# Performance work log

Hardware: AMD Instinct MI355X
Metric: run time of the kernel (lower is better)

Reference implementation:

```python
import jax, jax.numpy as jnp
import numpy as np

B, LC, LQ, D = 32, 2048, 256, 256


def setup_inputs() -> dict:
    key = jax.random.key(0)
    kc, kq, kcm, kqm, kw = jax.random.split(key, 5)
    context = jax.random.normal(kc, (B, LC, D), dtype=jnp.float32)
    query = jax.random.normal(kq, (B, LQ, D), dtype=jnp.float32)
    # True = masked (matches torch masked_fill semantics)
    context_mask = jax.random.randint(kcm, (B, LC), 0, 2).astype(bool)
    query_mask = jax.random.randint(kqm, (B, LQ), 0, 2).astype(bool)
    # nn.Linear(3*dim, 1, bias=False) weight, flattened to (3D,)
    w0 = jax.random.normal(kw, (3 * D,), dtype=jnp.float32) * (1.0 / np.sqrt(3 * D))
    return {"context": context, "query": query, "context_mask": context_mask,
            "query_mask": query_mask, "w0": w0}


def reference(context, query, context_mask, query_mask, w0):
    d = context.shape[-1]
    wc, wq, wm = w0[:d], w0[d:2 * d], w0[2 * d:]
    # trilinear sim: w0 . [c, q, c*q]  ==  c.wc + q.wq + (c*wm) q^T
    sc = context @ wc                                   # (B, Lc)
    sq = query @ wq                                     # (B, Lq)
    sim = sc[:, :, None] + sq[:, None, :] + jnp.einsum(
        'bcd,bqd->bcq', context * wm, query)            # (B, Lc, Lq)
    mask = context_mask[:, :, None] | query_mask[:, None, :]
    sim = jnp.where(mask, jnp.float32(-1e30), sim)
    S = jax.nn.softmax(sim, axis=-1)                    # row softmax over Lq
    SS = jax.nn.softmax(sim, axis=1)                    # col softmax over Lc
    S = jnp.nan_to_num(S)
    SS = jnp.nan_to_num(SS)
    A = jnp.einsum('bcq,bqd->bcd', S, query)            # (B, Lc, D)
    T = jnp.einsum('bkq,bkd->bqd', SS, context)         # SS^T @ context, (B, Lq, D)
    Bmat = jnp.einsum('bcq,bqd->bcd', S, T)             # (B, Lc, D)
    return (A, Bmat)
```

## Files before the change

### kernel.cpp

```cpp
#include <hip/hip_runtime.h>

#define B_  32
#define LC_ 2048
#define LQ_ 256
#define D_  256
#define NEGH (-30000.0f)
#define MASKF (-100000.0f)

typedef _Float16 f16;
typedef _Float16 f16x4 __attribute__((ext_vector_type(4)));
typedef _Float16 f16x8 __attribute__((ext_vector_type(8)));
typedef float    f32x4 __attribute__((ext_vector_type(4)));

__global__ __launch_bounds__(256) void k_prepq(
    const float* __restrict__ qry, const float* __restrict__ w0,
    const int* __restrict__ qmask,
    f16* __restrict__ qrywm16, float* __restrict__ sqm)
{
    const int lane = threadIdx.x & 63;
    const int wave = threadIdx.x >> 6;
    const int r = blockIdx.x * 4 + wave;
    float4 v = *(const float4*)(qry + (long long)r * D_ + lane * 4);
    float4 wm = *(const float4*)(w0 + 2 * D_ + lane * 4);
    f16x4 h;
    h[0] = (f16)(v.x * wm.x); h[1] = (f16)(v.y * wm.y);
    h[2] = (f16)(v.z * wm.z); h[3] = (f16)(v.w * wm.w);
    *(f16x4*)(qrywm16 + (long long)r * D_ + lane * 4) = h;
    float4 wq = *(const float4*)(w0 + D_ + lane * 4);
    float s = v.x*wq.x + v.y*wq.y + v.z*wq.z + v.w*wq.w;
    #pragma unroll
    for (int off = 32; off > 0; off >>= 1) s += __shfl_down(s, off, 64);
    if (lane == 0) sqm[r] = qmask[r] ? MASKF : s;
}

__global__ __launch_bounds__(256) void k_tq(
    const float* __restrict__ in, f16* __restrict__ out)
{
    __shared__ float tile[64 * 65];
    const int b = blockIdx.z;
    const int r0 = blockIdx.x * 64, c0 = blockIdx.y * 64;
    const int t = threadIdx.x;
    const float* ib = in + (long long)b * LQ_ * D_;
    #pragma unroll
    for (int p = 0; p < 4; ++p) {
        int r = (t >> 4) + p * 16;
        int cb = (t & 15) * 4;
        float4 v = *(const float4*)(ib + (long long)(r0 + r) * D_ + c0 + cb);
        tile[r * 65 + cb + 0] = v.x;
        tile[r * 65 + cb + 1] = v.y;
        tile[r * 65 + cb + 2] = v.z;
        tile[r * 65 + cb + 3] = v.w;
    }
    __syncthreads();
    f16* ob = out + (long long)b * 512 * LQ_;
    #pragma unroll
    for (int p = 0; p < 4; ++p) {
        int c = (t >> 4) + p * 16;
        int rb = (t & 15) * 4;
        f16x4 h;
        h[0] = (f16)tile[(rb + 0) * 65 + c];
        h[1] = (f16)tile[(rb + 1) * 65 + c];
        h[2] = (f16)tile[(rb + 2) * 65 + c];
        h[3] = (f16)tile[(rb + 3) * 65 + c];
        *(f16x4*)(ob + (long long)(c0 + c) * LQ_ + r0 + rb) = h;
    }
}

#define LDA1 40
__global__ __launch_bounds__(512, 4) void k_g1(
    const float* __restrict__ ctx, const f16* __restrict__ qrywm16,
    const float* __restrict__ w0, const int* __restrict__ cmask,
    const float* __restrict__ sqm,
    f16* __restrict__ ctxT16, f16* __restrict__ p16, f16* __restrict__ pT16,
    float* __restrict__ rowm, float* __restrict__ rowinvl,
    float* __restrict__ pm, float* __restrict__ pl)
{
    __shared__ f16 As[128 * LDA1];
    __shared__ f16 Bs[256 * LDA1];
    __shared__ float wc_s[256];
    __shared__ float scm_s[128];
    __shared__ float rowpm[4][128], rowps[4][128];
    __shared__ float colpm[2][256], colps[2][256];
    __shared__ float rowmax_s[128], colmax_s[256];
    const int b = blockIdx.z;
    const int c0 = blockIdx.x * 128;
    const int t = threadIdx.x, lane = t & 63, wv = t >> 6;
    const int wm_off = (wv >> 2) * 64, wn_off = (wv & 3) * 64;
    const float* Ab = ctx + ((long long)b * LC_ + c0) * D_;
    const f16* Bb = qrywm16 + (long long)b * LQ_ * D_;
    const int srow = t >> 2, scg = (t & 3) * 8;
    const int td = t & 31, tcc = t >> 5;
    if (t < 256) wc_s[t] = w0[t];
    __syncthreads();
    f32x4 acc[4][4] = {};
    float scdot = 0.f;
    for (int k0 = 0; k0 < D_; k0 += 32) {
        float4 a0 = *(const float4*)(Ab + (long long)srow * D_ + k0 + scg);
        float4 a1 = *(const float4*)(Ab + (long long)srow * D_ + k0 + scg + 4);
        f16x8 ha;
        ha[0] = (f16)a0.x; ha[1] = (f16)a0.y; ha[2] = (f16)a0.z; ha[3] = (f16)a0.w;
        ha[4] = (f16)a1.x; ha[5] = (f16)a1.y; ha[6] = (f16)a1.z; ha[7] = (f16)a1.w;
        scdot += a0.x * wc_s[k0 + scg + 0] + a0.y * wc_s[k0 + scg + 1]
               + a0.z * wc_s[k0 + scg + 2] + a0.w * wc_s[k0 + scg + 3]
               + a1.x * wc_s[k0 + scg + 4] + a1.y * wc_s[k0 + scg + 5]
               + a1.z * wc_s[k0 + scg + 6] + a1.w * wc_s[k0 + scg + 7];
        *(f16x8*)(As + srow * LDA1 + scg) = ha;
        *(f16x8*)(Bs + srow * LDA1 + scg) = *(const f16x8*)(Bb + (long long)srow * D_ + k0 + scg);
        *(f16x8*)(Bs + (srow + 128) * LDA1 + scg) = *(const f16x8*)(Bb + (long long)(srow + 128) * D_ + k0 + scg);
        __syncthreads();
        f16x8 af[4], bf[4];
        #pragma unroll
        for (int i = 0; i < 4; ++i)
            af[i] = *(const f16x8*)(As + (wm_off + i * 16 + (lane & 15)) * LDA1 + (lane >> 4) * 8);
        #pragma unroll
        for (int j = 0; j < 4; ++j)
            bf[j] = *(const f16x8*)(Bs + (wn_off + j * 16 + (lane & 15)) * LDA1 + (lane >> 4) * 8);
        #pragma unroll
        for (int i = 0; i < 4; ++i)
            #pragma unroll
            for (int j = 0; j < 4; ++j)
                acc[i][j] = __builtin_amdgcn_mfma_f32_16x16x32_f16(af[i], bf[j], acc[i][j], 0, 0, 0);
        {
            f16x8 hT;
            #pragma unroll
            for (int j = 0; j < 8; ++j)
                hT[j] = As[(tcc * 8 + j) * LDA1 + td];
            *(f16x8*)(ctxT16 + ((long long)b * D_ + k0 + td) * LC_ + c0 + tcc * 8) = hT;
        }
        __syncthreads();
    }
    scdot += __shfl_xor(scdot, 1, 64);
    scdot += __shfl_xor(scdot, 2, 64);
    if ((t & 3) == 0)
        scm_s[srow] = cmask[b * LC_ + c0 + srow] ? MASKF : scdot;
    __syncthreads();
    float sqv[4];
    #pragma unroll
    for (int j = 0; j < 4; ++j)
        sqv[j] = sqm[b * LQ_ + wn_off + j * 16 + (lane & 15)];
    float scv[4][4];
    #pragma unroll
    for (int i = 0; i < 4; ++i)
        #pragma unroll
        for (int r = 0; r < 4; ++r)
            scv[i][r] = scm_s[wm_off + i * 16 + (lane >> 4) * 4 + r];
    float rmax[4][4], cmax[4];
    #pragma unroll
    for (int i = 0; i < 4; ++i)
        #pragma unroll
        for (int r = 0; r < 4; ++r) rmax[i][r] = -INFINITY;
    #pragma unroll
    for (int j = 0; j < 4; ++j) cmax[j] = -INFINITY;
    #pragma unroll
    for (int i = 0; i < 4; ++i) {
        #pragma unroll
        for (int r = 0; r < 4; ++r) {
            #pragma unroll
            for (int j = 0; j < 4; ++j) {
                float val = fmaxf(acc[i][j][r] + scv[i][r] + sqv[j], NEGH);
                float vr = (float)(f16)val;
                rmax[i][r] = fmaxf(rmax[i][r], vr);
                cmax[j]    = fmaxf(cmax[j], vr);
            }
        }
    }
    #pragma unroll
    for (int i = 0; i < 4; ++i)
        #pragma unroll
        for (int r = 0; r < 4; ++r) {
            rmax[i][r] = fmaxf(rmax[i][r], __shfl_xor(rmax[i][r], 1, 64));
            rmax[i][r] = fmaxf(rmax[i][r], __shfl_xor(rmax[i][r], 2, 64));
            rmax[i][r] = fmaxf(rmax[i][r], __shfl_xor(rmax[i][r], 4, 64));
            rmax[i][r] = fmaxf(rmax[i][r], __shfl_xor(rmax[i][r], 8, 64));
        }
    #pragma unroll
    for (int j = 0; j < 4; ++j) {
        cmax[j] = fmaxf(cmax[j], __shfl_xor(cmax[j], 16, 64));
        cmax[j] = fmaxf(cmax[j], __shfl_xor(cmax[j], 32, 64));
    }
    if ((lane & 15) == 0) {
        #pragma unroll
        for (int i = 0; i < 4; ++i)
            #pragma unroll
            for (int r = 0; r < 4; ++r)
                rowpm[wv & 3][wm_off + i * 16 + (lane >> 4) * 4 + r] = rmax[i][r];
    }
    if (lane < 16) {
        #pragma unroll
        for (int j = 0; j < 4; ++j) colpm[wv >> 2][wn_off + j * 16 + lane] = cmax[j];
    }
    __syncthreads();
    if (t < 128)
        rowmax_s[t] = fmaxf(fmaxf(rowpm[0][t], rowpm[1][t]), fmaxf(rowpm[2][t], rowpm[3][t]));
    if (t < 256)
        colmax_s[t] = fmaxf(colpm[0][t], colpm[1][t]);
    __syncthreads();
    float rmf[4][4], cmf[4];
    #pragma unroll
    for (int i = 0; i < 4; ++i)
        #pragma unroll
        for (int r = 0; r < 4; ++r)
            rmf[i][r] = rowmax_s[wm_off + i * 16 + (lane >> 4) * 4 + r];
    #pragma unroll
    for (int j = 0; j < 4; ++j) cmf[j] = colmax_s[wn_off + j * 16 + (lane & 15)];
    float rsum[4][4] = {}, csum[4] = {};
    #pragma unroll
    for (int i = 0; i < 4; ++i) {
        #pragma unroll
        for (int r = 0; r < 4; ++r) {
            int c = c0 + wm_off + i * 16 + (lane >> 4) * 4 + r;
            f16* prow = p16 + ((long long)b * LC_ + c) * LQ_ + wn_off + (lane & 15);
            #pragma unroll
            for (int j = 0; j < 4; ++j) {
                int q = wn_off + j * 16 + (lane & 15);
                float val = fmaxf(acc[i][j][r] + scv[i][r] + sqv[j], NEGH);
                float vr = (float)(f16)val;
                float er = __expf(vr - rmf[i][r]);
                f16 hp = (f16)er;
                prow[j * 16] = hp;
                pT16[((long long)b * LQ_ + q) * LC_ + c] = hp;
                rsum[i][r] += er;
                csum[j]    += __expf(vr - cmf[j]);
            }
        }
    }
    #pragma unroll
    for (int i = 0; i < 4; ++i)
        #pragma unroll
        for (int r = 0; r < 4; ++r) {
            rsum[i][r] += __shfl_xor(rsum[i][r], 1, 64);
            rsum[i][r] += __shfl_xor(rsum[i][r], 2, 64);
            rsum[i][r] += __shfl_xor(rsum[i][r], 4, 64);
            rsum[i][r] += __shfl_xor(rsum[i][r], 8, 64);
        }
    #pragma unroll
    for (int j = 0; j < 4; ++j) {
        csum[j] += __shfl_xor(csum[j], 16, 64);
        csum[j] += __shfl_xor(csum[j], 32, 64);
    }
    if ((lane & 15) == 0) {
        #pragma unroll
        for (int i = 0; i < 4; ++i)
            #pragma unroll
            for (int r = 0; r < 4; ++r)
                rowps[wv & 3][wm_off + i * 16 + (lane >> 4) * 4 + r] = rsum[i][r];
    }
    if (lane < 16) {
        #pragma unroll
        for (int j = 0; j < 4; ++j) colps[wv >> 2][wn_off + j * 16 + lane] = csum[j];
    }
    __syncthreads();
    if (t < 128) {
        float l = rowps[0][t] + rowps[1][t] + rowps[2][t] + rowps[3][t];
        rowm[b * LC_ + c0 + t]    = rowmax_s[t];
        rowinvl[b * LC_ + c0 + t] = 1.0f / l;
    }
    if (t < 256) {
        int idx = (b * 16 + blockIdx.x) * LQ_ + t;
        pm[idx] = colmax_s[t];
        pl[idx] = colps[0][t] + colps[1][t];
    }
}

__global__ __launch_bounds__(256) void k_colreduce(
    const float* __restrict__ pm, const float* __restrict__ pl,
    float* __restrict__ colm, float* __restrict__ colinvl)
{
    const int col = blockIdx.x * 256 + threadIdx.x;
    const int b = col >> 8, q = col & 255;
    float M = -INFINITY, L = 0.f;
    for (int ch = 0; ch < 16; ++ch) {
        int idx = (b * 16 + ch) * LQ_ + q;
        float m = pm[idx], l = pl[idx];
        float nM = fmaxf(M, m);
        L = L * __expf(M - nM) + l * __expf(m - nM);
        M = nM;
    }
    colm[col] = M; colinvl[col] = 1.0f / L;
}

#define LDA3 72
#define G3SPLIT 4
#define G3CHUNK (LC_ / G3SPLIT)
__global__ __launch_bounds__(256) void k_g3(
    const f16* __restrict__ ctxT16, const f16* __restrict__ pT16,
    const float* __restrict__ rowm, const float* __restrict__ colm,
    float* __restrict__ Tpart)
{
    __shared__ f16 As[128 * LDA3];
    __shared__ f16 Bs[64 * LDA3];
    __shared__ float rowm_s[G3CHUNK];
    __shared__ float colm_s[64];
    const int b = blockIdx.x;
    const int combo = blockIdx.y;
    const int qt = combo & 3, dh = combo >> 2;
    const int q0 = qt * 64, d0 = dh * 128;
    const int cbeg = blockIdx.z * G3CHUNK;
    const int t = threadIdx.x, lane = t & 63, wv = t >> 6;
    const int wm_off = (wv >> 1) * 64, wn_off = (wv & 1) * 32;
    for (int i = t; i < G3CHUNK; i += 256) rowm_s[i] = rowm[b * LC_ + cbeg + i];
    if (t < 64) colm_s[t] = colm[b * LQ_ + q0 + t];
    __syncthreads();
    const f16* Ab = ctxT16 + ((long long)b * D_ + d0) * LC_;
    const f16* Pb = pT16 + ((long long)b * LQ_ + q0) * LC_;
    const int ar = t >> 3, acg = (t & 7) * 8;
    f32x4 acc[4][2] = {};
    f16x8 ha[4], hb[2];
    #pragma unroll
    for (int p = 0; p < 4; ++p)
        ha[p] = *(const f16x8*)(Ab + (long long)(ar + p * 32) * LC_ + cbeg + acg);
    #pragma unroll
    for (int p = 0; p < 2; ++p)
        hb[p] = *(const f16x8*)(Pb + (long long)(ar + p * 32) * LC_ + cbeg + acg);
    for (int c0 = cbeg; c0 < cbeg + G3CHUNK; c0 += 64) {
        #pragma unroll
        for (int p = 0; p < 4; ++p)
            *(f16x8*)(As + (ar + p * 32) * LDA3 + acg) = ha[p];
        #pragma unroll
        for (int p = 0; p < 2; ++p) {
            float cmq = colm_s[ar + p * 32];
            f16x8 e;
            if (cmq < -29000.f) {
                #pragma unroll
                for (int j = 0; j < 8; ++j) e[j] = (f16)1.0f;
            } else {
                #pragma unroll
                for (int j = 0; j < 8; ++j)
                    e[j] = (f16)((float)hb[p][j] * __expf(rowm_s[(c0 - cbeg) + acg + j] - cmq));
            }
            *(f16x8*)(Bs + (ar + p * 32) * LDA3 + acg) = e;
        }
        if (c0 + 64 < cbeg + G3CHUNK) {
            #pragma unroll
            for (int p = 0; p < 4; ++p)
                ha[p] = *(const f16x8*)(Ab + (long long)(ar + p * 32) * LC_ + c0 + 64 + acg);
            #pragma unroll
            for (int p = 0; p < 2; ++p)
                hb[p] = *(const f16x8*)(Pb + (long long)(ar + p * 32) * LC_ + c0 + 64 + acg);
        }
        __syncthreads();
        #pragma unroll
        for (int kk = 0; kk < 64; kk += 32) {
            f16x8 af[4], bf[2];
            #pragma unroll
            for (int i = 0; i < 4; ++i)
                af[i] = *(const f16x8*)(As + (wm_off + i * 16 + (lane & 15)) * LDA3 + kk + (lane >> 4) * 8);
            #pragma unroll
            for (int j = 0; j < 2; ++j)
                bf[j] = *(const f16x8*)(Bs + (wn_off + j * 16 + (lane & 15)) * LDA3 + kk + (lane >> 4) * 8);
            #pragma unroll
            for (int i = 0; i < 4; ++i)
                #pragma unroll
                for (int j = 0; j < 2; ++j)
                    acc[i][j] = __builtin_amdgcn_mfma_f32_16x16x32_f16(af[i], bf[j], acc[i][j], 0, 0, 0);
        }
        __syncthreads();
    }
    float* Tb = Tpart + ((long long)blockIdx.z * B_ + b) * (LQ_ * D_);
    #pragma unroll
    for (int i = 0; i < 4; ++i) {
        #pragma unroll
        for (int r = 0; r < 4; ++r) {
            int d = d0 + wm_off + i * 16 + (lane >> 4) * 4 + r;
            float* orow = Tb + (long long)d * LQ_ + q0 + wn_off + (lane & 15);
            #pragma unroll
            for (int j = 0; j < 2; ++j)
                orow[j * 16] = acc[i][j][r];
        }
    }
}

__global__ __launch_bounds__(256) void k_bnorm(
    const float* __restrict__ Tpart, const float* __restrict__ colinvl,
    f16* __restrict__ Bcat)
{
    const long long i4 = ((long long)blockIdx.x * 256 + threadIdx.x) * 4;
    const int q = (int)(i4 & 255);
    const int d = (int)((i4 >> 8) & 255);
    const int b = (int)(i4 >> 16);
    float4 s = *(const float4*)(Tpart + i4);
    #pragma unroll
    for (int p = 1; p < G3SPLIT; ++p) {
        float4 v = *(const float4*)(Tpart + (long long)p * (B_ * LQ_ * D_) + i4);
        s.x += v.x; s.y += v.y; s.z += v.z; s.w += v.w;
    }
    float4 ci = *(const float4*)(colinvl + b * LQ_ + q);
    f16x4 h;
    h[0] = (f16)(s.x * ci.x); h[1] = (f16)(s.y * ci.y);
    h[2] = (f16)(s.z * ci.z); h[3] = (f16)(s.w * ci.w);
    *(f16x4*)(Bcat + (long long)b * 512 * LQ_ + (long long)(256 + d) * LQ_ + q) = h;
}

__global__ __launch_bounds__(256, 4) void k_g23(
    const f16* __restrict__ p16, const float* __restrict__ rowinvl,
    const f16* __restrict__ Bcat,
    float* __restrict__ outA, float* __restrict__ outB)
{
    __shared__ f16 As[128 * LDA1];
    __shared__ f16 Bs[128 * LDA1];
    const int b = blockIdx.z;
    const int c0 = blockIdx.x * 128, n0 = blockIdx.y * 128;
    const int t = threadIdx.x, lane = t & 63, wv = t >> 6;
    const int wm_off = (wv >> 1) * 64, wn_off = (wv & 1) * 64;
    const f16* Ab = p16 + ((long long)b * LC_ + c0) * LQ_;
    const f16* Bb = Bcat + ((long long)b * 512 + n0) * LQ_;
    const int srow = t >> 2, scg = (t & 3) * 8;
    f32x4 acc[4][4] = {};
    f16x8 ha[2], hb[2];
    #pragma unroll
    for (int p = 0; p < 2; ++p) {
        int r = srow + p * 64;
        ha[p] = *(const f16x8*)(Ab + (long long)r * LQ_ + scg);
        hb[p] = *(const f16x8*)(Bb + (long long)r * LQ_ + scg);
    }
    for (int k0 = 0; k0 < LQ_; k0 += 32) {
        #pragma unroll
        for (int p = 0; p < 2; ++p) {
            int r = srow + p * 64;
            *(f16x8*)(As + r * LDA1 + scg) = ha[p];
            *(f16x8*)(Bs + r * LDA1 + scg) = hb[p];
        }
        if (k0 + 32 < LQ_) {
            #pragma unroll
            for (int p = 0; p < 2; ++p) {
                int r = srow + p * 64;
                ha[p] = *(const f16x8*)(Ab + (long long)r * LQ_ + k0 + 32 + scg);
                hb[p] = *(const f16x8*)(Bb + (long long)r * LQ_ + k0 + 32 + scg);
            }
        }
        __syncthreads();
        f16x8 af[4], bf[4];
        #pragma unroll
        for (int i = 0; i < 4; ++i)
            af[i] = *(const f16x8*)(As + (wm_off + i * 16 + (lane & 15)) * LDA1 + (lane >> 4) * 8);
        #pragma unroll
        for (int j = 0; j < 4; ++j)
            bf[j] = *(const f16x8*)(Bs + (wn_off + j * 16 + (lane & 15)) * LDA1 + (lane >> 4) * 8);
        #pragma unroll
        for (int i = 0; i < 4; ++i)
            #pragma unroll
            for (int j = 0; j < 4; ++j)
                acc[i][j] = __builtin_amdgcn_mfma_f32_16x16x32_f16(af[i], bf[j], acc[i][j], 0, 0, 0);
        __syncthreads();
    }
    float* outp = (n0 < 256) ? outA : outB;
    const int nbase = (n0 < 256) ? n0 : (n0 - 256);
    #pragma unroll
    for (int i = 0; i < 4; ++i) {
        #pragma unroll
        for (int r = 0; r < 4; ++r) {
            int c = c0 + wm_off + i * 16 + (lane >> 4) * 4 + r;
            float ri = rowinvl[b * LC_ + c];
            float* orow = outp + ((long long)b * LC_ + c) * D_ + nbase + wn_off + (lane & 15);
            #pragma unroll
            for (int j = 0; j < 4; ++j)
                orow[j * 16] = acc[i][j][r] * ri;
        }
    }
}

extern "C" void kernel_launch(void* const* d_in, const int* in_sizes, int n_in,
                              void* d_out, int out_size, void* d_ws, size_t ws_size,
                              hipStream_t stream) {
    const float* ctx   = (const float*)d_in[0];
    const float* qry   = (const float*)d_in[1];
    const int*   cmask = (const int*)d_in[2];
    const int*   qmask = (const int*)d_in[3];
    const float* w0    = (const float*)d_in[4];
    float* out = (float*)d_out;

    char* w = (char*)d_ws;
    float* sqm     = (float*)w;  w += (long long)8192 * 4;
    float* rowm    = (float*)w;  w += (long long)65536 * 4;
    float* rowinvl = (float*)w;  w += (long long)65536 * 4;
    float* colm    = (float*)w;  w += (long long)8192 * 4;
    float* colinvl = (float*)w;  w += (long long)8192 * 4;
    float* pm      = (float*)w;  w += (long long)524288 * 4;
    float* pl      = (float*)w;  w += (long long)524288 * 4;
    f16*   p16     = (f16*)w;    w += (long long)16777216 * 2;
    f16*   pT16    = (f16*)w;    w += (long long)16777216 * 2;
    f16*   ctxT16  = (f16*)w;    w += (long long)16777216 * 2;
    f16*   qrywm16 = (f16*)w;    w += (long long)2097152 * 2;
    f16*   Bcat    = (f16*)w;    w += (long long)4194304 * 2;
    float* Tpart   = (float*)w;  w += (long long)G3SPLIT * 2097152 * 4;

    k_prepq<<<2048, 256, 0, stream>>>(qry, w0, qmask, qrywm16, sqm);
    k_tq<<<dim3(4, 4, 32), 256, 0, stream>>>(qry, Bcat);
    k_g1<<<dim3(16, 1, 32), 512, 0, stream>>>(ctx, qrywm16, w0, cmask, sqm,
        ctxT16, p16, pT16, rowm, rowinvl, pm, pl);
    k_colreduce<<<32, 256, 0, stream>>>(pm, pl, colm, colinvl);
    k_g3<<<dim3(32, 8, G3SPLIT), 256, 0, stream>>>(ctxT16, pT16, rowm, colm, Tpart);
    k_bnorm<<<2048, 256, 0, stream>>>(Tpart, colinvl, Bcat);
    k_g23<<<dim3(16, 4, 32), 256, 0, stream>>>(p16, rowinvl, Bcat,
        out, out + (long long)B_ * LC_ * D_);
}
```

Measured before the change: 312.6 us.

## Enlarge g3 and g23 tiles to 512-thread blocks with swizzled 1D grids

k_g3 now covers a 128x128 output tile with 8 waves instead of 128x64 with 4 waves. k_g23 covers 256x256 with 8 waves, each holding an 8x4 MFMA accumulator grid. Both kernels move to a 1D grid with a block-index swizzle that spreads consecutive blocks across batches and splits. The aim is more data reuse per LDS load, fewer global reloads, and better cache locality. The cost is a much larger accumulator register footprint in k_g23 (128 floats per lane), which lowers occupancy and risks spilling, plus fewer, larger blocks.

```diff
diff --git a/kernel.cpp b/kernel.cpp
--- a/kernel.cpp
+++ b/kernel.cpp
@@ -282,43 +282,43 @@
 #define LDA3 72
 #define G3SPLIT 4
 #define G3CHUNK (LC_ / G3SPLIT)
-__global__ __launch_bounds__(256) void k_g3(
+__global__ __launch_bounds__(512) void k_g3(
     const f16* __restrict__ ctxT16, const f16* __restrict__ pT16,
     const float* __restrict__ rowm, const float* __restrict__ colm,
     float* __restrict__ Tpart)
 {
     __shared__ f16 As[128 * LDA3];
-    __shared__ f16 Bs[64 * LDA3];
+    __shared__ f16 Bs[128 * LDA3];
     __shared__ float rowm_s[G3CHUNK];
-    __shared__ float colm_s[64];
-    const int b = blockIdx.x;
-    const int combo = blockIdx.y;
-    const int qt = combo & 3, dh = combo >> 2;
-    const int q0 = qt * 64, d0 = dh * 128;
-    const int cbeg = blockIdx.z * G3CHUNK;
+    __shared__ float colm_s[128];
+    const int lin = blockIdx.x;
+    const int swz = (lin & 7) * 64 + (lin >> 3);
+    const int combo = swz & 3;
+    const int split = (swz >> 2) & 3;
+    const int b = swz >> 4;
+    const int qt = combo & 1, dh = combo >> 1;
+    const int q0 = qt * 128, d0 = dh * 128;
+    const int cbeg = split * G3CHUNK;
     const int t = threadIdx.x, lane = t & 63, wv = t >> 6;
-    const int wm_off = (wv >> 1) * 64, wn_off = (wv & 1) * 32;
-    for (int i = t; i < G3CHUNK; i += 256) rowm_s[i] = rowm[b * LC_ + cbeg + i];
-    if (t < 64) colm_s[t] = colm[b * LQ_ + q0 + t];
+    const int wm_off = (wv >> 2) * 64, wn_off = (wv & 3) * 32;
+    if (t < G3CHUNK) rowm_s[t] = rowm[b * LC_ + cbeg + t];
+    if (t < 128) colm_s[t] = colm[b * LQ_ + q0 + t];
     __syncthreads();
     const f16* Ab = ctxT16 + ((long long)b * D_ + d0) * LC_;
     const f16* Pb = pT16 + ((long long)b * LQ_ + q0) * LC_;
     const int ar = t >> 3, acg = (t & 7) * 8;
     f32x4 acc[4][2] = {};
-    f16x8 ha[4], hb[2];
-    #pragma unroll
-    for (int p = 0; p < 4; ++p)
-        ha[p] = *(const f16x8*)(Ab + (long long)(ar + p * 32) * LC_ + cbeg + acg);
-    #pragma unroll
-    for (int p = 0; p < 2; ++p)
-        hb[p] = *(const f16x8*)(Pb + (long long)(ar + p * 32) * LC_ + cbeg + acg);
+    f16x8 ha[2], hb[2];
+    #pragma unroll
+    for (int p = 0; p < 2; ++p) {
+        ha[p] = *(const f16x8*)(Ab + (long long)(ar + p * 64) * LC_ + cbeg + acg);
+        hb[p] = *(const f16x8*)(Pb + (long long)(ar + p * 64) * LC_ + cbeg + acg);
+    }
     for (int c0 = cbeg; c0 < cbeg + G3CHUNK; c0 += 64) {
         #pragma unroll
-        for (int p = 0; p < 4; ++p)
-            *(f16x8*)(As + (ar + p * 32) * LDA3 + acg) = ha[p];
-        #pragma unroll
         for (int p = 0; p < 2; ++p) {
-            float cmq = colm_s[ar + p * 32];
+            *(f16x8*)(As + (ar + p * 64) * LDA3 + acg) = ha[p];
+            float cmq = colm_s[ar + p * 64];
             f16x8 e;
             if (cmq < -29000.f) {
                 #pragma unroll
@@ -328,15 +328,14 @@
                 for (int j = 0; j < 8; ++j)
                     e[j] = (f16)((float)hb[p][j] * __expf(rowm_s[(c0 - cbeg) + acg + j] - cmq));
             }
-            *(f16x8*)(Bs + (ar + p * 32) * LDA3 + acg) = e;
+            *(f16x8*)(Bs + (ar + p * 64) * LDA3 + acg) = e;
         }
         if (c0 + 64 < cbeg + G3CHUNK) {
             #pragma unroll
-            for (int p = 0; p < 4; ++p)
-                ha[p] = *(const f16x8*)(Ab + (long long)(ar + p * 32) * LC_ + c0 + 64 + acg);
-            #pragma unroll
-            for (int p = 0; p < 2; ++p)
-                hb[p] = *(const f16x8*)(Pb + (long long)(ar + p * 32) * LC_ + c0 + 64 + acg);
+            for (int p = 0; p < 2; ++p) {
+                ha[p] = *(const f16x8*)(Ab + (long long)(ar + p * 64) * LC_ + c0 + 64 + acg);
+                hb[p] = *(const f16x8*)(Pb + (long long)(ar + p * 64) * LC_ + c0 + 64 + acg);
+            }
         }
         __syncthreads();
         #pragma unroll
@@ -356,7 +355,7 @@
         }
         __syncthreads();
     }
-    float* Tb = Tpart + ((long long)blockIdx.z * B_ + b) * (LQ_ * D_);
+    float* Tb = Tpart + ((long long)split * B_ + b) * (LQ_ * D_);
     #pragma unroll
     for (int i = 0; i < 4; ++i) {
         #pragma unroll
@@ -391,67 +390,71 @@
     *(f16x4*)(Bcat + (long long)b * 512 * LQ_ + (long long)(256 + d) * LQ_ + q) = h;
 }
 
-__global__ __launch_bounds__(256, 4) void k_g23(
+#define LDA23 40
+__global__ __launch_bounds__(512) void k_g23(
     const f16* __restrict__ p16, const float* __restrict__ rowinvl,
     const f16* __restrict__ Bcat,
     float* __restrict__ outA, float* __restrict__ outB)
 {
-    __shared__ f16 As[128 * LDA1];
-    __shared__ f16 Bs[128 * LDA1];
-    const int b = blockIdx.z;
-    const int c0 = blockIdx.x * 128, n0 = blockIdx.y * 128;
+    __shared__ f16 As[256 * LDA23];
+    __shared__ f16 Bs[256 * LDA23];
+    const int lin = blockIdx.x;
+    const int swz = (lin & 7) * 64 + (lin >> 3);
+    const int cx = swz & 7;
+    const int ny = (swz >> 3) & 1;
+    const int b  = swz >> 4;
+    const int c0 = cx * 256, n0 = ny * 256;
     const int t = threadIdx.x, lane = t & 63, wv = t >> 6;
-    const int wm_off = (wv >> 1) * 64, wn_off = (wv & 1) * 64;
+    const int wm_off = (wv >> 2) * 128;
+    const int wn_off = (wv & 3) * 64;
     const f16* Ab = p16 + ((long long)b * LC_ + c0) * LQ_;
     const f16* Bb = Bcat + ((long long)b * 512 + n0) * LQ_;
     const int srow = t >> 2, scg = (t & 3) * 8;
-    f32x4 acc[4][4] = {};
+    f32x4 acc[8][4] = {};
     f16x8 ha[2], hb[2];
     #pragma unroll
     for (int p = 0; p < 2; ++p) {
-        int r = srow + p * 64;
+        int r = srow + p * 128;
         ha[p] = *(const f16x8*)(Ab + (long long)r * LQ_ + scg);
         hb[p] = *(const f16x8*)(Bb + (long long)r * LQ_ + scg);
     }
     for (int k0 = 0; k0 < LQ_; k0 += 32) {
         #pragma unroll
         for (int p = 0; p < 2; ++p) {
-            int r = srow + p * 64;
-            *(f16x8*)(As + r * LDA1 + scg) = ha[p];
-            *(f16x8*)(Bs + r * LDA1 + scg) = hb[p];
+            int r = srow + p * 128;
+            *(f16x8*)(As + r * LDA23 + scg) = ha[p];
+            *(f16x8*)(Bs + r * LDA23 + scg) = hb[p];
         }
         if (k0 + 32 < LQ_) {
             #pragma unroll
             for (int p = 0; p < 2; ++p) {
-                int r = srow + p * 64;
+                int r = srow + p * 128;
                 ha[p] = *(const f16x8*)(Ab + (long long)r * LQ_ + k0 + 32 + scg);
                 hb[p] = *(const f16x8*)(Bb + (long long)r * LQ_ + k0 + 32 + scg);
             }
         }
         __syncthreads();
-        f16x8 af[4], bf[4];
-        #pragma unroll
-        for (int i = 0; i < 4; ++i)
-            af[i] = *(const f16x8*)(As + (wm_off + i * 16 + (lane & 15)) * LDA1 + (lane >> 4) * 8);
+        f16x8 bf[4];
         #pragma unroll
         for (int j = 0; j < 4; ++j)
-            bf[j] = *(const f16x8*)(Bs + (wn_off + j * 16 + (lane & 15)) * LDA1 + (lane >> 4) * 8);
-        #pragma unroll
-        for (int i = 0; i < 4; ++i)
+            bf[j] = *(const f16x8*)(Bs + (wn_off + j * 16 + (lane & 15)) * LDA23 + (lane >> 4) * 8);
+        #pragma unroll
+        for (int i = 0; i < 8; ++i) {
+            f16x8 af = *(const f16x8*)(As + (wm_off + i * 16 + (lane & 15)) * LDA23 + (lane >> 4) * 8);
             #pragma unroll
             for (int j = 0; j < 4; ++j)
-                acc[i][j] = __builtin_amdgcn_mfma_f32_16x16x32_f16(af[i], bf[j], acc[i][j], 0, 0, 0);
-        __syncthreads();
-    }
-    float* outp = (n0 < 256) ? outA : outB;
-    const int nbase = (n0 < 256) ? n0 : (n0 - 256);
-    #pragma unroll
-    for (int i = 0; i < 4; ++i) {
+                acc[i][j] = __builtin_amdgcn_mfma_f32_16x16x32_f16(af, bf[j], acc[i][j], 0, 0, 0);
+        }
+        __syncthreads();
+    }
+    float* outp = (n0 == 0) ? outA : outB;
+    #pragma unroll
+    for (int i = 0; i < 8; ++i) {
         #pragma unroll
         for (int r = 0; r < 4; ++r) {
             int c = c0 + wm_off + i * 16 + (lane >> 4) * 4 + r;
             float ri = rowinvl[b * LC_ + c];
-            float* orow = outp + ((long long)b * LC_ + c) * D_ + nbase + wn_off + (lane & 15);
+            float* orow = outp + ((long long)b * LC_ + c) * D_ + wn_off + (lane & 15);
             #pragma unroll
             for (int j = 0; j < 4; ++j)
                 orow[j * 16] = acc[i][j][r] * ri;
@@ -489,8 +492,8 @@
     k_g1<<<dim3(16, 1, 32), 512, 0, stream>>>(ctx, qrywm16, w0, cmask, sqm,
         ctxT16, p16, pT16, rowm, rowinvl, pm, pl);
     k_colreduce<<<32, 256, 0, stream>>>(pm, pl, colm, colinvl);
-    k_g3<<<dim3(32, 8, G3SPLIT), 256, 0, stream>>>(ctxT16, pT16, rowm, colm, Tpart);
+    k_g3<<<512, 512, 0, stream>>>(ctxT16, pT16, rowm, colm, Tpart);
     k_bnorm<<<2048, 256, 0, stream>>>(Tpart, colinvl, Bcat);
-    k_g23<<<dim3(16, 4, 32), 256, 0, stream>>>(p16, rowinvl, Bcat,
+    k_g23<<<512, 512, 0, stream>>>(p16, rowinvl, Bcat,
         out, out + (long long)B_ * LC_ * D_);
 }
```

Result: no change. 309.7 us (-0.9%).
